# Performance work log

Measured on AMD Instinct MI355X. Metric: run time of the kernel, lower is better.

## Reference

```python
import jax, jax.numpy as jnp
import numpy as np

T, H = 8192, 2048
E, K = 16, 4
I_MOE = 1408
I_SHARED = 5632
SCALE = 0.02  # keep activations numerically sane (source uses randn init)


def setup_inputs() -> dict:
    key = jax.random.key(0)
    ks = jax.random.split(key, 8)
    return {
        "hidden_states": jax.random.normal(ks[0], (T, H), jnp.float32),
        "router_w": jax.random.normal(ks[1], (E, H), jnp.float32) * SCALE,
        "gate_up_w": jax.random.normal(ks[2], (E, H, 2 * I_MOE), jnp.float32) * SCALE,
        "down_w": jax.random.normal(ks[3], (E, I_MOE, H), jnp.float32) * SCALE,
        "shared_gate_w": jax.random.normal(ks[4], (H, I_SHARED), jnp.float32) * SCALE,
        "shared_up_w": jax.random.normal(ks[5], (H, I_SHARED), jnp.float32) * SCALE,
        "shared_down_w": jax.random.normal(ks[6], (I_SHARED, H), jnp.float32) * SCALE,
        "shared_expert_gate_w": jax.random.normal(ks[7], (H, 1), jnp.float32) * SCALE,
    }


def reference(hidden_states, router_w, gate_up_w, down_w,
              shared_gate_w, shared_up_w, shared_down_w, shared_expert_gate_w):
    t, h = hidden_states.shape
    e = router_w.shape[0]
    # --- Router: fp32 logits -> softmax -> top-k ---
    logits = hidden_states.astype(jnp.float32) @ router_w.T            # [T, E]
    probs = jax.nn.softmax(logits, axis=-1)
    routing_weights, routing_indices = jax.lax.top_k(probs, K)         # [T, K]
    # --- Dispatch: replicate each token K times, sort replicas by expert ---
    flat_experts = routing_indices.reshape(-1)                          # [T*K]
    perm = jnp.argsort(flat_experts)                                    # stable sort
    dispatched = hidden_states[perm // K]                               # [T*K, H]
    group_sizes = jnp.bincount(flat_experts, length=e).astype(jnp.int32)
    # --- Grouped GEMM experts (SwiGLU) ---
    merged = jax.lax.ragged_dot(dispatched, gate_up_w, group_sizes)     # [T*K, 2I]
    gate, up = jnp.split(merged, 2, axis=-1)
    act = jax.nn.silu(gate) * up                                        # [T*K, I]
    expert_out = jax.lax.ragged_dot(act, down_w, group_sizes)           # [T*K, H]
    # --- Unpermute + weighted combine ---
    inv = jnp.argsort(perm)
    replica_out = expert_out[inv].reshape(t, K, h)                      # [T, K, H]
    out = jnp.einsum('tk,tkh->th', routing_weights, replica_out)
    # --- Shared expert with sigmoid gate ---
    shared = (jax.nn.silu(hidden_states @ shared_gate_w)
              * (hidden_states @ shared_up_w)) @ shared_down_w          # [T, H]
    g = jax.nn.sigmoid(hidden_states @ shared_expert_gate_w)            # [T, 1]
    return out + g * shared
```

## Files before the change

kernel.cpp:

```cpp
#include <hip/hip_runtime.h>
#include <hip/hip_bf16.h>

#define T_TOK 8192
#define H_DIM 2048
#define NE    16
#define TOPK  4
#define IMOE  1408
#define ISH   5632
#define TK    (T_TOK*TOPK)
#define MAXT256 ((TK/256)+NE)

typedef __bf16 bf16;
typedef __attribute__((ext_vector_type(8))) __bf16 bf16x8;
typedef __attribute__((ext_vector_type(4))) float  f32x4;

__device__ __forceinline__ void gload_lds16(const bf16* g, bf16* l) {
  __builtin_amdgcn_global_load_lds((const __attribute__((address_space(1))) void*)g,
                                   (__attribute__((address_space(3))) void*)l, 16, 0, 0);
}
#define MEMFENCE asm volatile("" ::: "memory")
#define BARRIER  do { MEMFENCE; __builtin_amdgcn_s_barrier(); MEMFENCE; } while (0)
#define VMCNT4   asm volatile("s_waitcnt vmcnt(4)" ::: "memory")

__global__ __launch_bounds__(256) void cvt_transpose64(const float* __restrict__ in,
                                                       bf16* __restrict__ out,
                                                       int R, int C,
                                                       size_t strideIn, size_t strideOut,
                                                       int split, int base_off) {
  __shared__ float tile[64][65];
  const float* inm = in + (size_t)blockIdx.z * strideIn;
  bf16* outm = out + (size_t)blockIdx.z * strideOut;
  int c0 = blockIdx.x * 64, r0 = blockIdx.y * 64;
  int tid = threadIdx.x;
  int rr = tid >> 4, cc4 = (tid & 15) * 4;
  #pragma unroll
  for (int i = 0; i < 4; ++i) {
    f32x4 v = __builtin_nontemporal_load(
        (const f32x4*)&inm[(size_t)(r0 + rr + i * 16) * C + c0 + cc4]);
    tile[rr + i * 16][cc4 + 0] = v.x;
    tile[rr + i * 16][cc4 + 1] = v.y;
    tile[rr + i * 16][cc4 + 2] = v.z;
    tile[rr + i * 16][cc4 + 3] = v.w;
  }
  __syncthreads();
  int r8 = (tid & 7) * 8;
  #pragma unroll
  for (int i = 0; i < 2; ++i) {
    int c = (tid >> 3) + i * 32;
    int co = c0 + c;
    int orow;
    if (split < 0) orow = co;
    else {
      int cl = co, o = base_off;
      if (cl >= split) { cl -= split; o += 128; }
      orow = ((cl >> 7) << 8) + o + (cl & 127);
    }
    bf16x8 v;
    #pragma unroll
    for (int j = 0; j < 8; ++j) v[j] = (bf16)tile[r8 + j][c];
    *(bf16x8*)&outm[(size_t)orow * R + r0 + r8] = v;
  }
}

__global__ void init_kernel(int* counts, int* fill) {
  int i = threadIdx.x;
  if (i < NE) { counts[i] = 0; fill[i] = 0; }
}

__global__ __launch_bounds__(256) void router_kernel(const float* __restrict__ X,
                                                     const float* __restrict__ Wr,
                                                     const float* __restrict__ wgate,
                                                     bf16* __restrict__ Xbf,
                                                     float* __restrict__ topk_w,
                                                     int* __restrict__ topk_idx,
                                                     float* __restrict__ gate_sig) {
  const int wv = threadIdx.x >> 6, lane = threadIdx.x & 63;
  const int t = blockIdx.x * 4 + wv;
  const float* x = X + (size_t)t * H_DIM;
  float xf[32];
  #pragma unroll
  for (int j = 0; j < 32; ++j) xf[j] = x[j * 64 + lane];
  #pragma unroll
  for (int j = 0; j < 32; ++j) Xbf[(size_t)t * H_DIM + j * 64 + lane] = (bf16)xf[j];

  double lg = 0.0;
  for (int e = 0; e < NE + 1; ++e) {
    const float* w = (e < NE) ? (Wr + (size_t)e * H_DIM) : wgate;
    double s0 = 0.0, s1 = 0.0;
    #pragma unroll
    for (int j = 0; j < 32; j += 2) {
      s0 += (double)xf[j] * (double)w[j * 64 + lane];
      s1 += (double)xf[j + 1] * (double)w[(j + 1) * 64 + lane];
    }
    double s = s0 + s1;
    #pragma unroll
    for (int off = 32; off; off >>= 1) s += __shfl_xor(s, off);
    if (lane == e) lg = s;
  }

  double v = (lane < NE) ? lg : -1e300;
  double m = v;
  #pragma unroll
  for (int off = 32; off; off >>= 1) m = fmax(m, __shfl_xor(m, off));
  double ev = (lane < NE) ? exp(v - m) : 0.0;
  double den = ev;
  #pragma unroll
  for (int off = 32; off; off >>= 1) den += __shfl_xor(den, off);

  double vv = v;
  int widx = 0; double wval = 0.0;
  for (int k = 0; k < TOPK; ++k) {
    double bv = vv; int bi = lane;
    #pragma unroll
    for (int off = 32; off; off >>= 1) {
      double ov = __shfl_xor(bv, off);
      int oi = __shfl_xor(bi, off);
      if (ov > bv || (ov == bv && oi < bi)) { bv = ov; bi = oi; }
    }
    double evb = __shfl(ev, bi);
    if (lane == k) { widx = bi; wval = evb / den; }
    if (lane == bi) vv = -1e300;
  }
  if (lane < TOPK) {
    topk_idx[t * TOPK + lane] = widx;
    topk_w[t * TOPK + lane] = (float)wval;
  }
  if (lane == NE) gate_sig[t] = (float)(1.0 / (1.0 + exp(-lg)));
}

__global__ __launch_bounds__(256) void hist_kernel(const int* __restrict__ tidx,
                                                   int* __restrict__ counts) {
  __shared__ int h[NE];
  if (threadIdx.x < NE) h[threadIdx.x] = 0;
  __syncthreads();
  int gid = blockIdx.x * 256 + threadIdx.x;
  atomicAdd(&h[tidx[gid]], 1);
  __syncthreads();
  if (threadIdx.x < NE) atomicAdd(&counts[threadIdx.x], h[threadIdx.x]);
}

__global__ void scan_kernel(const int* __restrict__ counts, int* __restrict__ offs,
                            int* __restrict__ fill, int* __restrict__ ttab,
                            int* __restrict__ ntl) {
  if (threadIdx.x != 0) return;
  int off = 0;
  for (int e = 0; e < NE; ++e) { offs[e] = off; off += counts[e]; fill[e] = 0; }
  offs[NE] = off;
  int n = 0;
  for (int e = 0; e < NE; ++e) {
    int cnt = counts[e], end_ = offs[e] + cnt;
    for (int m = 0; m < cnt; m += 256) {
      ttab[n * 3 + 0] = e;
      ttab[n * 3 + 1] = offs[e] + m;
      ttab[n * 3 + 2] = end_;
      ++n;
    }
  }
  *ntl = n;
}

__global__ __launch_bounds__(256) void scatter_kernel(const int* __restrict__ topk_idx,
                                                      const int* __restrict__ offs,
                                                      int* __restrict__ fill,
                                                      int* __restrict__ row_token,
                                                      int* __restrict__ row_pos) {
  __shared__ int wc[4][NE];
  __shared__ int wbase[4][NE];
  __shared__ int bbase[NE];
  const int tid = threadIdx.x, wv = tid >> 6, lane = tid & 63;
  const int gid = blockIdx.x * 256 + tid;
  const int e = topk_idx[gid];
  int rank = 0;
  #pragma unroll
  for (int ex = 0; ex < NE; ++ex) {
    unsigned long long b = __ballot(e == ex);
    if (e == ex) rank = __popcll(b & ((1ull << lane) - 1));
    if (lane == 0) wc[wv][ex] = __popcll(b);
  }
  __syncthreads();
  if (tid < NE) {
    int s = 0;
    #pragma unroll
    for (int w = 0; w < 4; ++w) { wbase[w][tid] = s; s += wc[w][tid]; }
    bbase[tid] = atomicAdd(&fill[tid], s);
  }
  __syncthreads();
  int pos = offs[e] + bbase[e] + wbase[wv][e] + rank;
  row_token[pos] = gid >> 2;
  row_pos[gid] = pos;
}

__device__ __forceinline__ void mfma_cluster(f32x4 (&a)[4][2], bf16x8 (&A)[4][2],
                                             bf16x8 (&B)[2][2]) {
  __builtin_amdgcn_s_setprio(1);
  #pragma unroll
  for (int m = 0; m < 4; ++m)
    #pragma unroll
    for (int n = 0; n < 2; ++n) {
      a[m][n] = __builtin_amdgcn_mfma_f32_16x16x32_bf16(A[m][0], B[n][0], a[m][n], 0, 0, 0);
      a[m][n] = __builtin_amdgcn_mfma_f32_16x16x32_bf16(A[m][1], B[n][1], a[m][n], 0, 0, 0);
    }
  __builtin_amdgcn_s_setprio(0);
}

__global__ __launch_bounds__(512, 2) void gemm256(
    const bf16* __restrict__ A, int lda,
    const bf16* __restrict__ B, size_t strideB, int Ktot,
    bf16* __restrict__ C, int ldc,
    const int* __restrict__ row_token,
    const int* __restrict__ tile_tab, const int* __restrict__ n_tiles,
    int Mdense, int fuse_swiglu) {
  const int gx = gridDim.x, gy = gridDim.y;
  int id = blockIdx.y * gx + blockIdx.x;
  int mt, nt;
  if ((gx & 7) == 0) {
    int oct = id / (8 * gy);
    int rem = id - oct * 8 * gy;
    mt = oct * 8 + (rem & 7);
    nt = rem >> 3;
  } else {
    mt = id % gx;
    nt = id / gx;
  }

  int e, row_start, row_end;
  if (tile_tab) {
    if (mt >= *n_tiles) return;
    e = tile_tab[mt * 3 + 0];
    row_start = tile_tab[mt * 3 + 1];
    row_end = tile_tab[mt * 3 + 2];
  } else {
    e = 0; row_start = mt * 256; row_end = Mdense;
  }
  const bf16* Bp = B + (size_t)e * strideB;

  __shared__ bf16 smA[2][2][8192];
  __shared__ bf16 smB[2][2][8192];

  const int tid = threadIdx.x;
  const int wave = tid >> 6;
  const int lane = tid & 63;

  unsigned aoff[2][2], boff[2][2];
  {
    int csrc = (((tid & 7) ^ ((tid >> 3) & 7)) << 3);
    #pragma unroll
    for (int h = 0; h < 2; ++h)
      #pragma unroll
      for (int j = 0; j < 2; ++j) {
        int rho = j * 64 + (tid >> 3);
        int r = row_start + h * 128 + rho;
        if (r > row_end - 1) r = row_end - 1;
        int sr = row_token ? row_token[r] : r;
        aoff[h][j] = (unsigned)sr * (unsigned)lda + (unsigned)csrc;
        boff[h][j] = (unsigned)(nt * 256 + h * 128 + rho) * (unsigned)Ktot + (unsigned)csrc;
      }
  }

  auto STAGE_A = [&](int bufi, int h, int tt) {
    gload_lds16(A + (size_t)(aoff[h][0] + (unsigned)tt * 64u), &smA[bufi][h][wave << 9]);
    gload_lds16(A + (size_t)(aoff[h][1] + (unsigned)tt * 64u), &smA[bufi][h][4096 + (wave << 9)]);
  };
  auto STAGE_B = [&](int bufi, int h, int tt) {
    gload_lds16(Bp + (size_t)(boff[h][0] + (unsigned)tt * 64u), &smB[bufi][h][wave << 9]);
    gload_lds16(Bp + (size_t)(boff[h][1] + (unsigned)tt * 64u), &smB[bufi][h][4096 + (wave << 9)]);
  };

  const int warow = ((wave >> 2) << 6) + (lane & 15);
  const int wbrow = ((wave & 3) << 5) + (lane & 15);
  const int q4 = lane >> 4;
  auto LDA_ = [&](int bufi, int h, int m, int kk) -> bf16x8 {
    int row = warow + m * 16;
    int c = (kk * 4 + q4) ^ (row & 7);
    return *(const bf16x8*)&smA[bufi][h][row * 64 + c * 8];
  };
  auto LDB_ = [&](int bufi, int h, int n, int kk) -> bf16x8 {
    int row = wbrow + n * 16;
    int c = (kk * 4 + q4) ^ (row & 7);
    return *(const bf16x8*)&smB[bufi][h][row * 64 + c * 8];
  };

  f32x4 acc[4][4][2];
  #pragma unroll
  for (int q = 0; q < 4; ++q)
    #pragma unroll
    for (int m = 0; m < 4; ++m)
      #pragma unroll
      for (int n = 0; n < 2; ++n) acc[q][m][n] = (f32x4){0.f, 0.f, 0.f, 0.f};

  bf16x8 Ar[4][2], Br0[2][2], Br1[2][2];

#define RD_A(BUF, H) do { \
    _Pragma("unroll") for (int m_ = 0; m_ < 4; ++m_) { \
      Ar[m_][0] = LDA_(BUF, H, m_, 0); Ar[m_][1] = LDA_(BUF, H, m_, 1); } } while (0)
#define RD_B(BUF, H, DST) do { \
    _Pragma("unroll") for (int n_ = 0; n_ < 2; ++n_) { \
      DST[n_][0] = LDB_(BUF, H, n_, 0); DST[n_][1] = LDB_(BUF, H, n_, 1); } } while (0)

#define DO_TILE(CB, NB, TS) do { \
     \
    RD_A(CB, 0); RD_B(CB, 0, Br0); \
    STAGE_A(NB, 0, TS); \
    BARRIER; \
    mfma_cluster(acc[0], Ar, Br0); \
    VMCNT4; \
    BARRIER; \
     \
    RD_B(CB, 1, Br1); \
    STAGE_B(NB, 0, TS); \
    BARRIER; \
    mfma_cluster(acc[1], Ar, Br1); \
    VMCNT4; \
    BARRIER; \
     \
    RD_A(CB, 1); \
    STAGE_B(NB, 1, TS); \
    BARRIER; \
    mfma_cluster(acc[2], Ar, Br1); \
    BARRIER; \
     \
    STAGE_A(NB, 1, TS); \
    mfma_cluster(acc[3], Ar, Br0); \
    VMCNT4; \
    BARRIER; \
  } while (0)

  STAGE_A(0, 0, 0); STAGE_B(0, 0, 0); STAGE_B(0, 1, 0); STAGE_A(0, 1, 0);
  VMCNT4; BARRIER;

  const int nk = Ktot >> 6;
  for (int it = 0; it < nk; it += 2) {
    const int ts1 = it + 1;
    const int ts2 = (it + 2 < nk) ? it + 2 : it + 1;
    DO_TILE(0, 1, ts1);
    DO_TILE(1, 0, ts2);
  }
#undef DO_TILE
#undef RD_A
#undef RD_B

  const int er = (lane >> 4) * 4;
  if (fuse_swiglu) {
    const int cb0 = nt * 128 + ((wave & 3) << 5) + (lane & 15);
    #pragma unroll
    for (int qi = 0; qi < 2; ++qi) {
      const int qg = qi ? 3 : 0, qu = qi ? 2 : 1;
      int rb = row_start + qi * 128 + ((wave >> 2) << 6) + er;
      #pragma unroll
      for (int m = 0; m < 4; ++m)
        #pragma unroll
        for (int n = 0; n < 2; ++n)
          #pragma unroll
          for (int j = 0; j < 4; ++j) {
            int r = rb + m * 16 + j;
            if (r < row_end) {
              float g = acc[qg][m][n][j];
              float u = acc[qu][m][n][j];
              float s = g / (1.f + __expf(-g));
              C[(size_t)r * ldc + cb0 + n * 16] = (bf16)(s * u);
            }
          }
    }
  } else {
    const int qr[4] = {0, 0, 1, 1}, qc[4] = {0, 1, 1, 0};
    #pragma unroll
    for (int q = 0; q < 4; ++q) {
      int rb = row_start + qr[q] * 128 + ((wave >> 2) << 6) + er;
      int cb0 = nt * 256 + qc[q] * 128 + ((wave & 3) << 5) + (lane & 15);
      #pragma unroll
      for (int m = 0; m < 4; ++m)
        #pragma unroll
        for (int n = 0; n < 2; ++n)
          #pragma unroll
          for (int j = 0; j < 4; ++j) {
            int r = rb + m * 16 + j;
            if (r < row_end) C[(size_t)r * ldc + cb0 + n * 16] = (bf16)acc[q][m][n][j];
          }
    }
  }
}

__global__ __launch_bounds__(256) void combine_kernel(const float* __restrict__ topk_w,
                                                      const int* __restrict__ row_pos,
                                                      const bf16* __restrict__ eout,
                                                      const bf16* __restrict__ shout,
                                                      const float* __restrict__ gate_sig,
                                                      float* __restrict__ out) {
  int t = blockIdx.x;
  float w0 = topk_w[t * 4 + 0], w1 = topk_w[t * 4 + 1];
  float w2 = topk_w[t * 4 + 2], w3 = topk_w[t * 4 + 3];
  size_t p0 = (size_t)row_pos[t * 4 + 0] * H_DIM;
  size_t p1 = (size_t)row_pos[t * 4 + 1] * H_DIM;
  size_t p2 = (size_t)row_pos[t * 4 + 2] * H_DIM;
  size_t p3 = (size_t)row_pos[t * 4 + 3] * H_DIM;
  float g = gate_sig[t];
  size_t tb = (size_t)t * H_DIM;
  size_t hb = (size_t)threadIdx.x * 8;
  bf16x8 a0 = *(const bf16x8*)&eout[p0 + hb];
  bf16x8 a1 = *(const bf16x8*)&eout[p1 + hb];
  bf16x8 a2 = *(const bf16x8*)&eout[p2 + hb];
  bf16x8 a3 = *(const bf16x8*)&eout[p3 + hb];
  bf16x8 sh = *(const bf16x8*)&shout[tb + hb];
  float r[8];
  #pragma unroll
  for (int j = 0; j < 8; ++j)
    r[j] = w0 * (float)a0[j] + w1 * (float)a1[j] + w2 * (float)a2[j]
         + w3 * (float)a3[j] + g * (float)sh[j];
  float4 o0 = {r[0], r[1], r[2], r[3]}, o1 = {r[4], r[5], r[6], r[7]};
  *(float4*)&out[tb + hb] = o0;
  *(float4*)&out[tb + hb + 4] = o1;
}

extern "C" void kernel_launch(void* const* d_in, const int* in_sizes, int n_in,
                              void* d_out, int out_size, void* d_ws, size_t ws_size,
                              hipStream_t stream) {
  const float* X   = (const float*)d_in[0];
  const float* Wr  = (const float*)d_in[1];
  const float* Wgu = (const float*)d_in[2];
  const float* Wd  = (const float*)d_in[3];
  const float* Wsg = (const float*)d_in[4];
  const float* Wsu = (const float*)d_in[5];
  const float* Wsd = (const float*)d_in[6];
  const float* Wge = (const float*)d_in[7];
  float* out = (float*)d_out;

  size_t off = 0;
  auto alloc = [&](size_t bytes) -> void* {
    void* p = (char*)d_ws + off;
    off += (bytes + 255) & ~(size_t)255;
    return p;
  };
  bf16* Xbf    = (bf16*)alloc((size_t)T_TOK * H_DIM * 2);
  bf16* WguT   = (bf16*)alloc((size_t)NE * 2 * IMOE * H_DIM * 2);
  bf16* WdT    = (bf16*)alloc((size_t)NE * H_DIM * IMOE * 2);
  bf16* WsguT  = (bf16*)alloc((size_t)2 * ISH * H_DIM * 2);
  bf16* WsdT   = (bf16*)alloc((size_t)H_DIM * ISH * 2);
  bf16* act    = (bf16*)alloc((size_t)TK * IMOE * 2);
  bf16* act_sh = (bf16*)alloc((size_t)T_TOK * ISH * 2);
  bf16* eout   = (bf16*)alloc((size_t)TK * H_DIM * 2);
  bf16* shout  = (bf16*)alloc((size_t)T_TOK * H_DIM * 2);
  float* tw    = (float*)alloc((size_t)T_TOK * TOPK * 4);
  int*   tidx  = (int*)alloc((size_t)T_TOK * TOPK * 4);
  float* gsig  = (float*)alloc((size_t)T_TOK * 4);
  int*   counts= (int*)alloc(64);
  int*   offs  = (int*)alloc(128);
  int*   fill  = (int*)alloc(64);
  int*   rowtok= (int*)alloc((size_t)TK * 4);
  int*   rowpos= (int*)alloc((size_t)TK * 4);
  int*   ttab  = (int*)alloc((size_t)MAXT256 * 3 * 4);
  int*   ntl   = (int*)alloc(64);
  if (off > ws_size) return;

  init_kernel<<<1, 32, 0, stream>>>(counts, fill);

  cvt_transpose64<<<dim3(H_DIM / 64, ISH / 64, 1), 256, 0, stream>>>(
      Wsd, WsdT, ISH, H_DIM, 0, 0, -1, 0);
  cvt_transpose64<<<dim3(ISH / 64, H_DIM / 64, 1), 256, 0, stream>>>(
      Wsg, WsguT, H_DIM, ISH, 0, 0, ISH, 0);
  cvt_transpose64<<<dim3(ISH / 64, H_DIM / 64, 1), 256, 0, stream>>>(
      Wsu, WsguT, H_DIM, ISH, 0, 0, ISH, 128);
  cvt_transpose64<<<dim3(H_DIM / 64, IMOE / 64, NE), 256, 0, stream>>>(
      Wd, WdT, IMOE, H_DIM, (size_t)IMOE * H_DIM, (size_t)IMOE * H_DIM, -1, 0);
  cvt_transpose64<<<dim3(2 * IMOE / 64, H_DIM / 64, NE), 256, 0, stream>>>(
      Wgu, WguT, H_DIM, 2 * IMOE, (size_t)H_DIM * 2 * IMOE, (size_t)H_DIM * 2 * IMOE, IMOE, 0);

  router_kernel<<<T_TOK / 4, 256, 0, stream>>>(X, Wr, Wge, Xbf, tw, tidx, gsig);
  hist_kernel<<<TK / 256, 256, 0, stream>>>(tidx, counts);
  scan_kernel<<<1, 64, 0, stream>>>(counts, offs, fill, ttab, ntl);
  scatter_kernel<<<TK / 256, 256, 0, stream>>>(tidx, offs, fill, rowtok, rowpos);

  gemm256<<<dim3(MAXT256, 2 * IMOE / 256), 512, 0, stream>>>(
      Xbf, H_DIM, WguT, (size_t)2 * IMOE * H_DIM, H_DIM,
      act, IMOE, rowtok, ttab, ntl, 0, 1);

  gemm256<<<dim3(MAXT256, H_DIM / 256), 512, 0, stream>>>(
      act, IMOE, WdT, (size_t)H_DIM * IMOE, IMOE,
      eout, H_DIM, nullptr, ttab, ntl, 0, 0);

  gemm256<<<dim3(T_TOK / 256, 2 * ISH / 256), 512, 0, stream>>>(
      Xbf, H_DIM, WsguT, 0, H_DIM,
      act_sh, ISH, nullptr, nullptr, nullptr, T_TOK, 1);
  gemm256<<<dim3(T_TOK / 256, H_DIM / 256), 512, 0, stream>>>(
      act_sh, ISH, WsdT, 0, ISH,
      shout, H_DIM, nullptr, nullptr, nullptr, T_TOK, 0);

  combine_kernel<<<T_TOK, 256, 0, stream>>>(tw, rowpos, eout, shout, gsig, out);
}
```

Before: 1.447 ms.

## Deepen GEMM prefetch pipeline to stage loads further ahead

```diff
diff --git a/kernel.cpp b/kernel.cpp
--- a/kernel.cpp
+++ b/kernel.cpp
@@ -20,7 +20,7 @@
 }
 #define MEMFENCE asm volatile("" ::: "memory")
 #define BARRIER  do { MEMFENCE; __builtin_amdgcn_s_barrier(); MEMFENCE; } while (0)
-#define VMCNT4   asm volatile("s_waitcnt vmcnt(4)" ::: "memory")
+#define VMCNT6   asm volatile("s_waitcnt vmcnt(6)" ::: "memory")
 
 __global__ __launch_bounds__(256) void cvt_transpose64(const float* __restrict__ in,
                                                        bf16* __restrict__ out,
@@ -297,43 +297,46 @@
     _Pragma("unroll") for (int n_ = 0; n_ < 2; ++n_) { \
       DST[n_][0] = LDB_(BUF, H, n_, 0); DST[n_][1] = LDB_(BUF, H, n_, 1); } } while (0)
 
-#define DO_TILE(CB, NB, TS) do { \
+#define DO_TILE(CB, NB, TS1, TS2) do { \
      \
     RD_A(CB, 0); RD_B(CB, 0, Br0); \
-    STAGE_A(NB, 0, TS); \
+    STAGE_A(NB, 1, TS1); \
     BARRIER; \
     mfma_cluster(acc[0], Ar, Br0); \
-    VMCNT4; \
     BARRIER; \
      \
     RD_B(CB, 1, Br1); \
-    STAGE_B(NB, 0, TS); \
+    STAGE_A(CB, 0, TS2); \
     BARRIER; \
     mfma_cluster(acc[1], Ar, Br1); \
-    VMCNT4; \
     BARRIER; \
      \
     RD_A(CB, 1); \
-    STAGE_B(NB, 1, TS); \
+    STAGE_B(CB, 0, TS2); \
     BARRIER; \
     mfma_cluster(acc[2], Ar, Br1); \
     BARRIER; \
      \
-    STAGE_A(NB, 1, TS); \
+    STAGE_B(CB, 1, TS2); \
     mfma_cluster(acc[3], Ar, Br0); \
-    VMCNT4; \
+    VMCNT6; \
     BARRIER; \
   } while (0)
 
+  const int nk = Ktot >> 6;
   STAGE_A(0, 0, 0); STAGE_B(0, 0, 0); STAGE_B(0, 1, 0); STAGE_A(0, 1, 0);
-  VMCNT4; BARRIER;
-
-  const int nk = Ktot >> 6;
+  {
+    int t1 = (1 < nk) ? 1 : 0;
+    STAGE_A(1, 0, t1); STAGE_B(1, 0, t1); STAGE_B(1, 1, t1);
+  }
+  VMCNT6; BARRIER;
+
   for (int it = 0; it < nk; it += 2) {
-    const int ts1 = it + 1;
-    const int ts2 = (it + 2 < nk) ? it + 2 : it + 1;
-    DO_TILE(0, 1, ts1);
-    DO_TILE(1, 0, ts2);
+    int ts1 = (it + 1 < nk) ? it + 1 : nk - 1;
+    int ts2 = (it + 2 < nk) ? it + 2 : nk - 1;
+    int ts3 = (it + 3 < nk) ? it + 3 : nk - 1;
+    DO_TILE(0, 1, ts1, ts2);
+    DO_TILE(1, 0, ts2, ts3);
   }
 #undef DO_TILE
 #undef RD_A
```

Result: slower. 1.477 ms (+2.1%).

## Switch GEMM to 32x32x16 MFMA and co-launch routed and shared GEMMs

Applied to the files above, without the earlier changes.

```diff
diff --git a/kernel.cpp b/kernel.cpp
--- a/kernel.cpp
+++ b/kernel.cpp
@@ -11,8 +11,9 @@
 #define MAXT256 ((TK/256)+NE)
 
 typedef __bf16 bf16;
-typedef __attribute__((ext_vector_type(8))) __bf16 bf16x8;
-typedef __attribute__((ext_vector_type(4))) float  f32x4;
+typedef __attribute__((ext_vector_type(8)))  __bf16 bf16x8;
+typedef __attribute__((ext_vector_type(4)))  float  f32x4;
+typedef __attribute__((ext_vector_type(16))) float  f32x16;
 
 __device__ __forceinline__ void gload_lds16(const bf16* g, bf16* l) {
   __builtin_amdgcn_global_load_lds((const __attribute__((address_space(1))) void*)g,
@@ -190,28 +191,30 @@
   row_pos[gid] = pos;
 }
 
-__device__ __forceinline__ void mfma_cluster(f32x4 (&a)[4][2], bf16x8 (&A)[4][2],
-                                             bf16x8 (&B)[2][2]) {
+__device__ __forceinline__ void mfma_cluster32(f32x16 (&a)[2], bf16x8 (&A)[2][4],
+                                               bf16x8 (&B)[4]) {
   __builtin_amdgcn_s_setprio(1);
   #pragma unroll
-  for (int m = 0; m < 4; ++m)
-    #pragma unroll
-    for (int n = 0; n < 2; ++n) {
-      a[m][n] = __builtin_amdgcn_mfma_f32_16x16x32_bf16(A[m][0], B[n][0], a[m][n], 0, 0, 0);
-      a[m][n] = __builtin_amdgcn_mfma_f32_16x16x32_bf16(A[m][1], B[n][1], a[m][n], 0, 0, 0);
-    }
+  for (int ks = 0; ks < 4; ++ks)
+    #pragma unroll
+    for (int m = 0; m < 2; ++m)
+      a[m] = __builtin_amdgcn_mfma_f32_32x32x16_bf16(A[m][ks], B[ks], a[m], 0, 0, 0);
   __builtin_amdgcn_s_setprio(0);
 }
 
-__global__ __launch_bounds__(512, 2) void gemm256(
-    const bf16* __restrict__ A, int lda,
-    const bf16* __restrict__ B, size_t strideB, int Ktot,
-    bf16* __restrict__ C, int ldc,
-    const int* __restrict__ row_token,
-    const int* __restrict__ tile_tab, const int* __restrict__ n_tiles,
-    int Mdense, int fuse_swiglu) {
-  const int gx = gridDim.x, gy = gridDim.y;
-  int id = blockIdx.y * gx + blockIdx.x;
+struct GArgs {
+  const bf16* A; const bf16* B; bf16* C;
+  const int* row_token; const int* tile_tab; const int* n_tiles;
+  size_t strideB;
+  int lda, Ktot, ldc, Mdense, gx, gy;
+};
+
+__global__ __launch_bounds__(512, 2) void gemm256(GArgs ga, GArgs gb, int nblk0,
+                                                  int fuse_swiglu) {
+  GArgs g; int id;
+  if ((int)blockIdx.x < nblk0) { g = ga; id = blockIdx.x; }
+  else { g = gb; id = blockIdx.x - nblk0; }
+  const int gx = g.gx, gy = g.gy;
   int mt, nt;
   if ((gx & 7) == 0) {
     int oct = id / (8 * gy);
@@ -224,15 +227,18 @@
   }
 
   int e, row_start, row_end;
-  if (tile_tab) {
-    if (mt >= *n_tiles) return;
-    e = tile_tab[mt * 3 + 0];
-    row_start = tile_tab[mt * 3 + 1];
-    row_end = tile_tab[mt * 3 + 2];
+  if (g.tile_tab) {
+    if (mt >= *g.n_tiles) return;
+    e = g.tile_tab[mt * 3 + 0];
+    row_start = g.tile_tab[mt * 3 + 1];
+    row_end = g.tile_tab[mt * 3 + 2];
   } else {
-    e = 0; row_start = mt * 256; row_end = Mdense;
-  }
-  const bf16* Bp = B + (size_t)e * strideB;
+    e = 0; row_start = mt * 256; row_end = g.Mdense;
+  }
+  const bf16* Ap = g.A;
+  const bf16* Bp = g.B + (size_t)e * g.strideB;
+  const int lda = g.lda, Ktot = g.Ktot, ldc = g.ldc;
+  bf16* C = g.C;
 
   __shared__ bf16 smA[2][2][8192];
   __shared__ bf16 smB[2][2][8192];
@@ -251,76 +257,74 @@
         int rho = j * 64 + (tid >> 3);
         int r = row_start + h * 128 + rho;
         if (r > row_end - 1) r = row_end - 1;
-        int sr = row_token ? row_token[r] : r;
+        int sr = g.row_token ? g.row_token[r] : r;
         aoff[h][j] = (unsigned)sr * (unsigned)lda + (unsigned)csrc;
         boff[h][j] = (unsigned)(nt * 256 + h * 128 + rho) * (unsigned)Ktot + (unsigned)csrc;
       }
   }
 
   auto STAGE_A = [&](int bufi, int h, int tt) {
-    gload_lds16(A + (size_t)(aoff[h][0] + (unsigned)tt * 64u), &smA[bufi][h][wave << 9]);
-    gload_lds16(A + (size_t)(aoff[h][1] + (unsigned)tt * 64u), &smA[bufi][h][4096 + (wave << 9)]);
+    gload_lds16(Ap + (size_t)(aoff[h][0] + (unsigned)tt * 64u), &smA[bufi][h][wave << 9]);
+    gload_lds16(Ap + (size_t)(aoff[h][1] + (unsigned)tt * 64u), &smA[bufi][h][4096 + (wave << 9)]);
   };
   auto STAGE_B = [&](int bufi, int h, int tt) {
     gload_lds16(Bp + (size_t)(boff[h][0] + (unsigned)tt * 64u), &smB[bufi][h][wave << 9]);
     gload_lds16(Bp + (size_t)(boff[h][1] + (unsigned)tt * 64u), &smB[bufi][h][4096 + (wave << 9)]);
   };
 
-  const int warow = ((wave >> 2) << 6) + (lane & 15);
-  const int wbrow = ((wave & 3) << 5) + (lane & 15);
-  const int q4 = lane >> 4;
-  auto LDA_ = [&](int bufi, int h, int m, int kk) -> bf16x8 {
-    int row = warow + m * 16;
-    int c = (kk * 4 + q4) ^ (row & 7);
+  const int warow = ((wave >> 2) << 6) + (lane & 31);
+  const int wbrow = ((wave & 3) << 5) + (lane & 31);
+  const int q5 = lane >> 5;
+  auto LDA_ = [&](int bufi, int h, int m, int ks) -> bf16x8 {
+    int row = warow + m * 32;
+    int c = (ks * 2 + q5) ^ (row & 7);
     return *(const bf16x8*)&smA[bufi][h][row * 64 + c * 8];
   };
-  auto LDB_ = [&](int bufi, int h, int n, int kk) -> bf16x8 {
-    int row = wbrow + n * 16;
-    int c = (kk * 4 + q4) ^ (row & 7);
-    return *(const bf16x8*)&smB[bufi][h][row * 64 + c * 8];
+  auto LDB_ = [&](int bufi, int h, int ks) -> bf16x8 {
+    int c = (ks * 2 + q5) ^ (wbrow & 7);
+    return *(const bf16x8*)&smB[bufi][h][wbrow * 64 + c * 8];
   };
 
-  f32x4 acc[4][4][2];
+  f32x16 acc[4][2];
   #pragma unroll
   for (int q = 0; q < 4; ++q)
     #pragma unroll
-    for (int m = 0; m < 4; ++m)
-      #pragma unroll
-      for (int n = 0; n < 2; ++n) acc[q][m][n] = (f32x4){0.f, 0.f, 0.f, 0.f};
-
-  bf16x8 Ar[4][2], Br0[2][2], Br1[2][2];
+    for (int m = 0; m < 2; ++m) acc[q][m] = (f32x16)(0.0f);
+
+  bf16x8 Ar[2][4], Br0[4], Br1[4];
 
 #define RD_A(BUF, H) do { \
-    _Pragma("unroll") for (int m_ = 0; m_ < 4; ++m_) { \
-      Ar[m_][0] = LDA_(BUF, H, m_, 0); Ar[m_][1] = LDA_(BUF, H, m_, 1); } } while (0)
+    _Pragma("unroll") for (int m_ = 0; m_ < 2; ++m_) \
+      _Pragma("unroll") for (int k_ = 0; k_ < 4; ++k_) \
+        Ar[m_][k_] = LDA_(BUF, H, m_, k_); } while (0)
 #define RD_B(BUF, H, DST) do { \
-    _Pragma("unroll") for (int n_ = 0; n_ < 2; ++n_) { \
-      DST[n_][0] = LDB_(BUF, H, n_, 0); DST[n_][1] = LDB_(BUF, H, n_, 1); } } while (0)
+    _Pragma("unroll") for (int k_ = 0; k_ < 4; ++k_) \
+      DST[k_] = LDB_(BUF, H, k_); } while (0)
 
 #define DO_TILE(CB, NB, TS) do { \
      \
     RD_A(CB, 0); RD_B(CB, 0, Br0); \
     STAGE_A(NB, 0, TS); \
     BARRIER; \
-    mfma_cluster(acc[0], Ar, Br0); \
+    mfma_cluster32(acc[0], Ar, Br0); \
     VMCNT4; \
     BARRIER; \
      \
     RD_B(CB, 1, Br1); \
     STAGE_B(NB, 0, TS); \
     BARRIER; \
-    mfma_cluster(acc[1], Ar, Br1); \
+    mfma_cluster32(acc[1], Ar, Br1); \
     VMCNT4; \
     BARRIER; \
      \
     RD_A(CB, 1); \
     STAGE_B(NB, 1, TS); \
     BARRIER; \
-    mfma_cluster(acc[2], Ar, Br1); \
+    mfma_cluster32(acc[2], Ar, Br1); \
     BARRIER; \
      \
     STAGE_A(NB, 1, TS); \
-    mfma_cluster(acc[3], Ar, Br0); \
+    mfma_cluster32(acc[3], Ar, Br0); \
     VMCNT4; \
     BARRIER; \
   } while (0)
@@ -339,43 +343,39 @@
 #undef RD_A
 #undef RD_B
 
-  const int er = (lane >> 4) * 4;
+  const int er = (lane >> 5) << 2;
   if (fuse_swiglu) {
-    const int cb0 = nt * 128 + ((wave & 3) << 5) + (lane & 15);
+    const int cb0 = nt * 128 + ((wave & 3) << 5) + (lane & 31);
     #pragma unroll
     for (int qi = 0; qi < 2; ++qi) {
       const int qg = qi ? 3 : 0, qu = qi ? 2 : 1;
       int rb = row_start + qi * 128 + ((wave >> 2) << 6) + er;
       #pragma unroll
-      for (int m = 0; m < 4; ++m)
+      for (int m = 0; m < 2; ++m)
         #pragma unroll
-        for (int n = 0; n < 2; ++n)
-          #pragma unroll
-          for (int j = 0; j < 4; ++j) {
-            int r = rb + m * 16 + j;
-            if (r < row_end) {
-              float g = acc[qg][m][n][j];
-              float u = acc[qu][m][n][j];
-              float s = g / (1.f + __expf(-g));
-              C[(size_t)r * ldc + cb0 + n * 16] = (bf16)(s * u);
-            }
+        for (int reg = 0; reg < 16; ++reg) {
+          int r = rb + m * 32 + (reg & 3) + ((reg >> 2) << 3);
+          if (r < row_end) {
+            float gg = acc[qg][m][reg];
+            float uu = acc[qu][m][reg];
+            float s = gg / (1.f + __expf(-gg));
+            C[(size_t)r * ldc + cb0] = (bf16)(s * uu);
           }
+        }
     }
   } else {
     const int qr[4] = {0, 0, 1, 1}, qc[4] = {0, 1, 1, 0};
     #pragma unroll
     for (int q = 0; q < 4; ++q) {
       int rb = row_start + qr[q] * 128 + ((wave >> 2) << 6) + er;
-      int cb0 = nt * 256 + qc[q] * 128 + ((wave & 3) << 5) + (lane & 15);
+      int cb0 = nt * 256 + qc[q] * 128 + ((wave & 3) << 5) + (lane & 31);
       #pragma unroll
-      for (int m = 0; m < 4; ++m)
+      for (int m = 0; m < 2; ++m)
         #pragma unroll
-        for (int n = 0; n < 2; ++n)
-          #pragma unroll
-          for (int j = 0; j < 4; ++j) {
-            int r = rb + m * 16 + j;
-            if (r < row_end) C[(size_t)r * ldc + cb0 + n * 16] = (bf16)acc[q][m][n][j];
-          }
+        for (int reg = 0; reg < 16; ++reg) {
+          int r = rb + m * 32 + (reg & 3) + ((reg >> 2) << 3);
+          if (r < row_end) C[(size_t)r * ldc + cb0] = (bf16)acc[q][m][reg];
+        }
     }
   }
 }
@@ -469,20 +469,35 @@
   scan_kernel<<<1, 64, 0, stream>>>(counts, offs, fill, ttab, ntl);
   scatter_kernel<<<TK / 256, 256, 0, stream>>>(tidx, offs, fill, rowtok, rowpos);
 
-  gemm256<<<dim3(MAXT256, 2 * IMOE / 256), 512, 0, stream>>>(
-      Xbf, H_DIM, WguT, (size_t)2 * IMOE * H_DIM, H_DIM,
-      act, IMOE, rowtok, ttab, ntl, 0, 1);
-
-  gemm256<<<dim3(MAXT256, H_DIM / 256), 512, 0, stream>>>(
-      act, IMOE, WdT, (size_t)H_DIM * IMOE, IMOE,
-      eout, H_DIM, nullptr, ttab, ntl, 0, 0);
-
-  gemm256<<<dim3(T_TOK / 256, 2 * ISH / 256), 512, 0, stream>>>(
-      Xbf, H_DIM, WsguT, 0, H_DIM,
-      act_sh, ISH, nullptr, nullptr, nullptr, T_TOK, 1);
-  gemm256<<<dim3(T_TOK / 256, H_DIM / 256), 512, 0, stream>>>(
-      act_sh, ISH, WsdT, 0, ISH,
-      shout, H_DIM, nullptr, nullptr, nullptr, T_TOK, 0);
+  GArgs g1;
+  g1.A = Xbf; g1.B = WguT; g1.C = act;
+  g1.row_token = rowtok; g1.tile_tab = ttab; g1.n_tiles = ntl;
+  g1.strideB = (size_t)2 * IMOE * H_DIM;
+  g1.lda = H_DIM; g1.Ktot = H_DIM; g1.ldc = IMOE; g1.Mdense = 0;
+  g1.gx = MAXT256; g1.gy = 2 * IMOE / 256;
+  GArgs gsg;
+  gsg.A = Xbf; gsg.B = WsguT; gsg.C = act_sh;
+  gsg.row_token = nullptr; gsg.tile_tab = nullptr; gsg.n_tiles = nullptr;
+  gsg.strideB = 0;
+  gsg.lda = H_DIM; gsg.Ktot = H_DIM; gsg.ldc = ISH; gsg.Mdense = T_TOK;
+  gsg.gx = T_TOK / 256; gsg.gy = 2 * ISH / 256;
+  int nb1 = g1.gx * g1.gy;
+  gemm256<<<nb1 + gsg.gx * gsg.gy, 512, 0, stream>>>(g1, gsg, nb1, 1);
+
+  GArgs g2;
+  g2.A = act; g2.B = WdT; g2.C = eout;
+  g2.row_token = nullptr; g2.tile_tab = ttab; g2.n_tiles = ntl;
+  g2.strideB = (size_t)H_DIM * IMOE;
+  g2.lda = IMOE; g2.Ktot = IMOE; g2.ldc = H_DIM; g2.Mdense = 0;
+  g2.gx = MAXT256; g2.gy = H_DIM / 256;
+  GArgs gsd;
+  gsd.A = act_sh; gsd.B = WsdT; gsd.C = shout;
+  gsd.row_token = nullptr; gsd.tile_tab = nullptr; gsd.n_tiles = nullptr;
+  gsd.strideB = 0;
+  gsd.lda = ISH; gsd.Ktot = ISH; gsd.ldc = H_DIM; gsd.Mdense = T_TOK;
+  gsd.gx = T_TOK / 256; gsd.gy = H_DIM / 256;
+  int nb2 = g2.gx * g2.gy;
+  gemm256<<<nb2 + gsd.gx * gsd.gy, 512, 0, stream>>>(g2, gsd, nb2, 0);
 
   combine_kernel<<<T_TOK, 256, 0, stream>>>(tw, rowpos, eout, shout, gsig, out);
 }
```

Result: slower. 1.628 ms (+12.5%).

## Merge MoE and shared-expert GEMMs into single launches over a combined grid

Applied to the files above, without the earlier changes.

```diff
diff --git a/kernel.cpp b/kernel.cpp
--- a/kernel.cpp
+++ b/kernel.cpp
@@ -203,15 +203,19 @@
   __builtin_amdgcn_s_setprio(0);
 }
 
-__global__ __launch_bounds__(512, 2) void gemm256(
-    const bf16* __restrict__ A, int lda,
-    const bf16* __restrict__ B, size_t strideB, int Ktot,
-    bf16* __restrict__ C, int ldc,
-    const int* __restrict__ row_token,
-    const int* __restrict__ tile_tab, const int* __restrict__ n_tiles,
-    int Mdense, int fuse_swiglu) {
-  const int gx = gridDim.x, gy = gridDim.y;
-  int id = blockIdx.y * gx + blockIdx.x;
+struct GArgs {
+  const bf16* A; const bf16* B; bf16* C;
+  const int* row_token; const int* tile_tab; const int* n_tiles;
+  size_t strideB;
+  int lda, Ktot, ldc, Mdense, gx, gy;
+};
+
+__global__ __launch_bounds__(512, 2) void gemm256(GArgs ga, GArgs gb, int nblk0,
+                                                  int fuse_swiglu) {
+  GArgs g; int id;
+  if ((int)blockIdx.x < nblk0) { g = ga; id = blockIdx.x; }
+  else { g = gb; id = blockIdx.x - nblk0; }
+  const int gx = g.gx, gy = g.gy;
   int mt, nt;
   if ((gx & 7) == 0) {
     int oct = id / (8 * gy);
@@ -224,15 +228,18 @@
   }
 
   int e, row_start, row_end;
-  if (tile_tab) {
-    if (mt >= *n_tiles) return;
-    e = tile_tab[mt * 3 + 0];
-    row_start = tile_tab[mt * 3 + 1];
-    row_end = tile_tab[mt * 3 + 2];
+  if (g.tile_tab) {
+    if (mt >= *g.n_tiles) return;
+    e = g.tile_tab[mt * 3 + 0];
+    row_start = g.tile_tab[mt * 3 + 1];
+    row_end = g.tile_tab[mt * 3 + 2];
   } else {
-    e = 0; row_start = mt * 256; row_end = Mdense;
-  }
-  const bf16* Bp = B + (size_t)e * strideB;
+    e = 0; row_start = mt * 256; row_end = g.Mdense;
+  }
+  const bf16* Ap = g.A;
+  const bf16* Bp = g.B + (size_t)e * g.strideB;
+  const int lda = g.lda, Ktot = g.Ktot, ldc = g.ldc;
+  bf16* C = g.C;
 
   __shared__ bf16 smA[2][2][8192];
   __shared__ bf16 smB[2][2][8192];
@@ -251,15 +258,15 @@
         int rho = j * 64 + (tid >> 3);
         int r = row_start + h * 128 + rho;
         if (r > row_end - 1) r = row_end - 1;
-        int sr = row_token ? row_token[r] : r;
+        int sr = g.row_token ? g.row_token[r] : r;
         aoff[h][j] = (unsigned)sr * (unsigned)lda + (unsigned)csrc;
         boff[h][j] = (unsigned)(nt * 256 + h * 128 + rho) * (unsigned)Ktot + (unsigned)csrc;
       }
   }
 
   auto STAGE_A = [&](int bufi, int h, int tt) {
-    gload_lds16(A + (size_t)(aoff[h][0] + (unsigned)tt * 64u), &smA[bufi][h][wave << 9]);
-    gload_lds16(A + (size_t)(aoff[h][1] + (unsigned)tt * 64u), &smA[bufi][h][4096 + (wave << 9)]);
+    gload_lds16(Ap + (size_t)(aoff[h][0] + (unsigned)tt * 64u), &smA[bufi][h][wave << 9]);
+    gload_lds16(Ap + (size_t)(aoff[h][1] + (unsigned)tt * 64u), &smA[bufi][h][4096 + (wave << 9)]);
   };
   auto STAGE_B = [&](int bufi, int h, int tt) {
     gload_lds16(Bp + (size_t)(boff[h][0] + (unsigned)tt * 64u), &smB[bufi][h][wave << 9]);
@@ -354,10 +361,10 @@
           for (int j = 0; j < 4; ++j) {
             int r = rb + m * 16 + j;
             if (r < row_end) {
-              float g = acc[qg][m][n][j];
-              float u = acc[qu][m][n][j];
-              float s = g / (1.f + __expf(-g));
-              C[(size_t)r * ldc + cb0 + n * 16] = (bf16)(s * u);
+              float g0 = acc[qg][m][n][j];
+              float u0 = acc[qu][m][n][j];
+              float s = g0 / (1.f + __expf(-g0));
+              C[(size_t)r * ldc + cb0 + n * 16] = (bf16)(s * u0);
             }
           }
     }
@@ -469,20 +476,35 @@
   scan_kernel<<<1, 64, 0, stream>>>(counts, offs, fill, ttab, ntl);
   scatter_kernel<<<TK / 256, 256, 0, stream>>>(tidx, offs, fill, rowtok, rowpos);
 
-  gemm256<<<dim3(MAXT256, 2 * IMOE / 256), 512, 0, stream>>>(
-      Xbf, H_DIM, WguT, (size_t)2 * IMOE * H_DIM, H_DIM,
-      act, IMOE, rowtok, ttab, ntl, 0, 1);
-
-  gemm256<<<dim3(MAXT256, H_DIM / 256), 512, 0, stream>>>(
-      act, IMOE, WdT, (size_t)H_DIM * IMOE, IMOE,
-      eout, H_DIM, nullptr, ttab, ntl, 0, 0);
-
-  gemm256<<<dim3(T_TOK / 256, 2 * ISH / 256), 512, 0, stream>>>(
-      Xbf, H_DIM, WsguT, 0, H_DIM,
-      act_sh, ISH, nullptr, nullptr, nullptr, T_TOK, 1);
-  gemm256<<<dim3(T_TOK / 256, H_DIM / 256), 512, 0, stream>>>(
-      act_sh, ISH, WsdT, 0, ISH,
-      shout, H_DIM, nullptr, nullptr, nullptr, T_TOK, 0);
+  GArgs g1;
+  g1.A = Xbf; g1.B = WguT; g1.C = act;
+  g1.row_token = rowtok; g1.tile_tab = ttab; g1.n_tiles = ntl;
+  g1.strideB = (size_t)2 * IMOE * H_DIM;
+  g1.lda = H_DIM; g1.Ktot = H_DIM; g1.ldc = IMOE; g1.Mdense = 0;
+  g1.gx = MAXT256; g1.gy = 2 * IMOE / 256;
+  GArgs gsg;
+  gsg.A = Xbf; gsg.B = WsguT; gsg.C = act_sh;
+  gsg.row_token = nullptr; gsg.tile_tab = nullptr; gsg.n_tiles = nullptr;
+  gsg.strideB = 0;
+  gsg.lda = H_DIM; gsg.Ktot = H_DIM; gsg.ldc = ISH; gsg.Mdense = T_TOK;
+  gsg.gx = T_TOK / 256; gsg.gy = 2 * ISH / 256;
+  int nb1 = g1.gx * g1.gy;
+  gemm256<<<nb1 + gsg.gx * gsg.gy, 512, 0, stream>>>(g1, gsg, nb1, 1);
+
+  GArgs g2;
+  g2.A = act; g2.B = WdT; g2.C = eout;
+  g2.row_token = nullptr; g2.tile_tab = ttab; g2.n_tiles = ntl;
+  g2.strideB = (size_t)H_DIM * IMOE;
+  g2.lda = IMOE; g2.Ktot = IMOE; g2.ldc = H_DIM; g2.Mdense = 0;
+  g2.gx = MAXT256; g2.gy = H_DIM / 256;
+  GArgs gsd;
+  gsd.A = act_sh; gsd.B = WsdT; gsd.C = shout;
+  gsd.row_token = nullptr; gsd.tile_tab = nullptr; gsd.n_tiles = nullptr;
+  gsd.strideB = 0;
+  gsd.lda = ISH; gsd.Ktot = ISH; gsd.ldc = H_DIM; gsd.Mdense = T_TOK;
+  gsd.gx = T_TOK / 256; gsd.gy = H_DIM / 256;
+  int nb2 = g2.gx * g2.gy;
+  gemm256<<<nb2 + gsd.gx * gsd.gy, 512, 0, stream>>>(g2, gsd, nb2, 0);
 
   combine_kernel<<<T_TOK, 256, 0, stream>>>(tw, rowpos, eout, shout, gsig, out);
 }
```

After: 1.445 ms. About the same (-0.1%).
